# Optimization experiments

Hardware: AMD Instinct MI355X
Metric: run time of the kernel (lower is better)

## Reference

```python
import jax, jax.numpy as jnp
import numpy as np

B, N, E, Dh, L = 64, 128, 1024, 300, 2  # batch, num_utter, emb_dim, hidden_dim, gnn_layers


def gru_cell(x, h, wih, whh, bih, bhh):
    # torch.nn.GRUCell math; gate order r, z, n
    gi = x @ wih.T + bih
    gh = h @ whh.T + bhh
    ir, iz, inn = jnp.split(gi, 3, axis=-1)
    hr, hz, hn = jnp.split(gh, 3, axis=-1)
    r = jax.nn.sigmoid(ir + hr)
    z = jax.nn.sigmoid(iz + hz)
    n = jnp.tanh(inn + r * hn)
    return (1.0 - z) * n + z * h


def dag_layer(Hl, mask, wg, bg, cwih, cwhh, cbih, cbhh, pwih, pwhh, pbih, pbhh):
    # Hl: (B,N,Dh); mask: (B,N,N) strict-causal DAG adjacency (float 0/1)
    wq, wk = wg[:Dh], wg[Dh:]  # GatLinear: Linear(2*Dh, 1) split over [Q; K]
    x0 = Hl[:, 0]
    z0 = jnp.zeros_like(x0)
    C0 = gru_cell(x0, z0, cwih, cwhh, cbih, cbhh)  # grus_c(H0, hx=None)
    P0 = gru_cell(z0, x0, pwih, pwhh, pbih, pbhh)  # grus_p(M=0, H0)
    buf0 = jnp.zeros_like(Hl).at[:, 0].set(C0 + P0)

    xs = (jnp.swapaxes(Hl[:, 1:], 0, 1),      # (N-1,B,Dh)
          jnp.swapaxes(mask[:, 1:], 0, 1),    # (N-1,B,N)
          jnp.arange(1, Hl.shape[1]))

    def step(buf, inp):
        x, m, i = inp  # x:(B,Dh), m:(B,N) allows only positions j<i with adj==1
        alpha = (x @ wq)[:, None] + buf @ wk + bg        # (B,N) additive score
        alpha = alpha - (1.0 - m) * 1e30                 # mask_logic
        w = jax.nn.softmax(alpha, axis=-1)
        M = jnp.einsum('bn,bnd->bd', w, buf)             # attn_sum over history H1
        C = gru_cell(x, M, cwih, cwhh, cbih, cbhh)       # grus_c(H_i, M)
        P = gru_cell(M, x, pwih, pwhh, pbih, pbhh)       # grus_p(M, H_i)
        return buf.at[:, i].set(C + P), None

    buf, _ = jax.lax.scan(step, buf0, xs)
    return buf


def setup_inputs():
    key = jax.random.key(0)
    ks = jax.random.split(key, 16)
    features = jax.random.normal(ks[0], (B, N, E), jnp.float32)
    adj = jax.random.randint(ks[1], (B, N, N), 0, 2, dtype=jnp.int32)
    idx = jnp.arange(1, N)
    adj = adj.at[:, idx, idx - 1].set(1)  # every utterance links to its predecessor (valid DAG)
    s_mask = jax.random.randint(ks[2], (B, N, N), 0, 2, dtype=jnp.int32)
    s_mask_onehot = jax.nn.one_hot(s_mask, 2, dtype=jnp.int32)
    lengths = jnp.full((B,), N, dtype=jnp.int32)
    s = 0.05
    return {
        'features': features,
        'fc1_w': jax.random.normal(ks[3], (E, Dh), jnp.float32) * s,
        'fc1_b': jnp.zeros((Dh,), jnp.float32),
        'gat_w': jax.random.normal(ks[4], (L, 2 * Dh), jnp.float32) * s,
        'gat_b': jnp.zeros((L,), jnp.float32),
        'gc_wih': jax.random.normal(ks[5], (L, 3 * Dh, Dh), jnp.float32) * s,
        'gc_whh': jax.random.normal(ks[6], (L, 3 * Dh, Dh), jnp.float32) * s,
        'gc_bih': jnp.zeros((L, 3 * Dh), jnp.float32),
        'gc_bhh': jnp.zeros((L, 3 * Dh), jnp.float32),
        'gp_wih': jax.random.normal(ks[7], (L, 3 * Dh, Dh), jnp.float32) * s,
        'gp_whh': jax.random.normal(ks[8], (L, 3 * Dh, Dh), jnp.float32) * s,
        'gp_bih': jnp.zeros((L, 3 * Dh), jnp.float32),
        'gp_bhh': jnp.zeros((L, 3 * Dh), jnp.float32),
        'adj': adj,
        's_mask': s_mask,
        's_mask_onehot': s_mask_onehot,
        'lengths': lengths,
    }


def reference(features, fc1_w, fc1_b, gat_w, gat_b, gc_wih, gc_whh, gc_bih, gc_bhh,
              gp_wih, gp_whh, gp_bih, gp_bhh, adj, s_mask, s_mask_onehot, lengths):
    H0 = jax.nn.relu(features @ fc1_w + fc1_b)                 # (B,N,Dh)
    causal = jnp.tril(jnp.ones((N, N), features.dtype), k=-1)  # strictly past (j<i)
    mask = adj.astype(features.dtype) * causal                 # adj[:, i, :i]
    Hs = [H0]
    Hl = H0
    for l in range(L):
        Hl = dag_layer(Hl, mask, gat_w[l], gat_b[l],
                       gc_wih[l], gc_whh[l], gc_bih[l], gc_bhh[l],
                       gp_wih[l], gp_whh[l], gp_bih[l], gp_bhh[l])
        Hs.append(Hl)
    Hs.append(features)
    # nodal_att_type=None -> attentive_node_features is identity; module returns H
    return jnp.concatenate(Hs, axis=2)  # (B,N,Dh*(L+1)+E)
```

## Files before the change

kernel.cpp:

```cpp
#include <hip/hip_runtime.h>
#include <hip/hip_fp16.h>

#define B_   64
#define NB   128
#define E_   1024
#define DH   300
#define G3   900
#define G6   1800
#define OUTD 1924
#define SLICES 4
#define PK_STRIDE 1800
#define MROW 160
#define BROWS 1856

typedef _Float16 h2raw __attribute__((ext_vector_type(2)));

__device__ __forceinline__ float dot2f(unsigned int m2, unsigned int w, float acc) {
    h2raw a, b;
    __builtin_memcpy(&a, &m2, 4);
    __builtin_memcpy(&b, &w, 4);
    return __builtin_amdgcn_fdot2(a, b, acc, false);
}

__device__ __forceinline__ unsigned int packh2(float x, float y) {
    __half2 h;
    h.x = __float2half_rn(x);
    h.y = __float2half_rn(y);
    unsigned int u;
    __builtin_memcpy(&u, &h, 4);
    return u;
}

__device__ __forceinline__ float sigmoidf_(float x) { return 1.f / (1.f + __expf(-x)); }
__device__ __forceinline__ float tanh_fast(float x) { return 1.f - 2.f / (__expf(2.f * x) + 1.f); }

__global__ __launch_bounds__(256)
void copy_feat(const float* __restrict__ f, float* __restrict__ out) {
    const long id = (long)blockIdx.x * 256 + threadIdx.x;
    const long r = id >> 8;
    const int  c = (int)(id & 255);
    const float4 v = ((const float4*)(f + r * E_))[c];
    ((float4*)(out + r * OUTD + 3 * DH))[c] = v;
}

__global__ __launch_bounds__(256)
void pack2(const float* __restrict__ gc_whh, const float* __restrict__ gp_wih,
           unsigned int* __restrict__ dst) {
    const int id = blockIdx.x * 256 + threadIdx.x;
    if (id >= 2 * 150 * PK_STRIDE) return;
    const int l   = id / (150 * PK_STRIDE);
    const int rem = id % (150 * PK_STRIDE);
    const int kp  = rem / PK_STRIDE;
    const int R   = rem % PK_STRIDE;
    const int mat = R / G3;
    const int o   = R % G3;
    const float* W = (mat ? gp_wih : gc_whh) + (long)l * G3 * DH;
    const float2 v = *(const float2*)(W + (long)o * DH + 2 * kp);
    dst[id] = packh2(v.x, v.y);
}

__global__ __launch_bounds__(256)
void pack_af(const float* __restrict__ src, unsigned int* __restrict__ dst) {
    const long id = (long)blockIdx.x * 256 + threadIdx.x;
    const long r = id >> 9;
    const int kp = (int)(id & 511);
    const float2 v = *(const float2*)(src + r * E_ + 2 * kp);
    dst[id] = packh2(v.x, v.y);
}

__global__ __launch_bounds__(256)
void pack_bf(const float* __restrict__ W, unsigned int* __restrict__ dst) {
    const int id = blockIdx.x * 256 + threadIdx.x;
    const int n = id >> 9;
    const int kp = id & 511;
    unsigned int u = 0u;
    if (n < DH) u = packh2(W[(2 * kp) * DH + n], W[(2 * kp + 1) * DH + n]);
    dst[id] = u;
}

__global__ __launch_bounds__(256)
void pack_bw2(const float* __restrict__ Wc, const float* __restrict__ Wp,
              unsigned int* __restrict__ dst) {
    const int id = blockIdx.x * 256 + threadIdx.x;
    if (id >= 2 * BROWS * 160) return;
    const int l   = id / (BROWS * 160);
    const int rem = id % (BROWS * 160);
    const int n   = rem / 160;
    const int kp  = rem % 160;
    unsigned int u = 0u;
    if (n < G6 && kp < 150) {
        const float* W = (n < G3 ? Wc : Wp) + (long)l * G3 * DH;
        const int o = (n < G3) ? n : n - G3;
        const float2 v = *(const float2*)(W + (long)o * DH + 2 * kp);
        u = packh2(v.x, v.y);
    }
    dst[id] = u;
}

template<int RELU, int PACKOUT>
__global__ __launch_bounds__(256)
void gemm_h16(const unsigned int* __restrict__ APK, int ldap,
              const unsigned int* __restrict__ BPK, int ldbp,
              const float* __restrict__ bias1, const float* __restrict__ bias2, int bsplit,
              float* __restrict__ C, int ldc,
              unsigned int* __restrict__ CPK, int ldcp,
              int N, int KP)
{
    __shared__ __align__(16) unsigned int As[16][132];
    __shared__ __align__(16) unsigned int Bs[16][68];
    const int tid = threadIdx.x;
    const int m0 = blockIdx.y * 128;
    const int n0 = blockIdx.x * 64;
    const int tx = tid & 15, ty = tid >> 4;
    const int am = tid >> 1, ak8 = (tid & 1) * 8;
    const int bn = tid >> 2, bk4 = (tid & 3) * 4;

    float acc[8][4] = {{0.f}};
    const unsigned int* ap = APK + (long)(m0 + am) * ldap + ak8;
    const unsigned int* bp = BPK + (long)(n0 + bn) * ldbp + bk4;

    for (int kp0 = 0; kp0 < KP; kp0 += 16) {
        const uint4 a0 = *(const uint4*)(ap + kp0);
        const uint4 a1 = *(const uint4*)(ap + kp0 + 4);
        const uint4 bq = *(const uint4*)(bp + kp0);
        As[ak8 + 0][am] = a0.x; As[ak8 + 1][am] = a0.y;
        As[ak8 + 2][am] = a0.z; As[ak8 + 3][am] = a0.w;
        As[ak8 + 4][am] = a1.x; As[ak8 + 5][am] = a1.y;
        As[ak8 + 6][am] = a1.z; As[ak8 + 7][am] = a1.w;
        Bs[bk4 + 0][bn] = bq.x; Bs[bk4 + 1][bn] = bq.y;
        Bs[bk4 + 2][bn] = bq.z; Bs[bk4 + 3][bn] = bq.w;
        __syncthreads();
        #pragma unroll
        for (int kp = 0; kp < 16; ++kp) {
            const uint4 aA = *(const uint4*)&As[kp][ty * 8];
            const uint4 aB = *(const uint4*)&As[kp][ty * 8 + 4];
            const uint4 bb = *(const uint4*)&Bs[kp][tx * 4];
            const unsigned int av[8] = {aA.x, aA.y, aA.z, aA.w, aB.x, aB.y, aB.z, aB.w};
            const unsigned int bv[4] = {bb.x, bb.y, bb.z, bb.w};
            #pragma unroll
            for (int ii = 0; ii < 8; ++ii)
                #pragma unroll
                for (int jj = 0; jj < 4; ++jj)
                    acc[ii][jj] = dot2f(av[ii], bv[jj], acc[ii][jj]);
        }
        __syncthreads();
    }

    const int gn0 = n0 + tx * 4;
    #pragma unroll
    for (int ii = 0; ii < 8; ++ii) {
        const int gm = m0 + ty * 8 + ii;
        float* cp = C + (long)gm * ldc + gn0;
        if (gn0 + 3 < N) {
            const float* bb4 = (gn0 < bsplit) ? bias1 + gn0 : bias2 + (gn0 - bsplit);
            const float4 bb = *(const float4*)bb4;
            float4 o;
            o.x = acc[ii][0] + bb.x; o.y = acc[ii][1] + bb.y;
            o.z = acc[ii][2] + bb.z; o.w = acc[ii][3] + bb.w;
            if (RELU) { o.x = fmaxf(o.x, 0.f); o.y = fmaxf(o.y, 0.f); o.z = fmaxf(o.z, 0.f); o.w = fmaxf(o.w, 0.f); }
            *(float4*)cp = o;
            if (PACKOUT) {
                unsigned int* pk = CPK + (long)gm * ldcp + (gn0 >> 1);
                pk[0] = packh2(o.x, o.y);
                pk[1] = packh2(o.z, o.w);
            }
        } else if (gn0 < N) {
            for (int jj = 0; jj < 4; ++jj) {
                const int gn = gn0 + jj;
                if (gn < N) {
                    float v = acc[ii][jj] + ((gn < bsplit) ? bias1[gn] : bias2[gn - bsplit]);
                    if (RELU) v = fmaxf(v, 0.f);
                    cp[jj] = v;
                }
            }
        }
    }
}

__global__ __launch_bounds__(512, 2)
void scan14(float* __restrict__ out,
            const float* __restrict__ GG,
            const unsigned int* __restrict__ PK2L,
            const float* __restrict__ cbhh,
            const float* __restrict__ pbih,
            const int* __restrict__ adj,
            const float* __restrict__ wk,
            unsigned long long* __restrict__ TBL,
            unsigned int* __restrict__ APKN,
            int l)
{
    extern __shared__ unsigned int histp[];
    __shared__ float wsm2[NB];
    __shared__ float betas[NB];
    __shared__ float Mlds[DH];
    __shared__ __align__(16) unsigned int M2[152];
    __shared__ float gmv[456];
    __shared__ float mx2s, S_pres;

    const int tid = threadIdx.x;
    const int lane = tid & 63;
    const int wid = tid >> 6;
    const int b = blockIdx.x & 63;
    const int k = blockIdx.x >> 6;
    const int swk = (k == 3) ? 72 : 76;

    float* outb = out + (long)b * NB * OUTD;
    const float* xcol = outb + l * DH;
    float* ycol = outb + (l + 1) * DH;
    const float* ggb = GG + (long)b * NB * G6;
    const int* adjb = adj + b * NB * NB;
    unsigned long long* mb = TBL + (long)b * NB * MROW;
    unsigned int* mb32 = (unsigned int*)mb;

    if (tid < 152) M2[tid] = 0u;

    const int D = 76 * k + ((tid < swk) ? tid : 0);
    const float cb0 = cbhh[D], cb1 = cbhh[DH + D], cb2 = cbhh[2 * DH + D];
    const float pb0 = pbih[D], pb1 = pbih[DH + D], pb2 = pbih[2 * DH + D];
    const float wkD = wk[D];

    const int ROWS = 6 * swk;
    int R;
    {
        const int t = (tid < ROWS) ? tid : 0;
        const int d = t % swk;
        const int r = t / swk;
        R = (r / 3) * G3 + (r % 3) * DH + 76 * k + d;
    }
    unsigned int w[152];
    #pragma unroll
    for (int j = 0; j < 150; ++j) w[j] = PK2L[j * PK_STRIDE + R];
    w[150] = 0u; w[151] = 0u;

    __syncthreads();

    const bool isv = (tid >= 256) && (tid < 406);
    const int vt = tid - 256;

    for (int i = 0; i < NB; ++i) {
        float gi0 = 0, gi1 = 0, gi2 = 0, gp0 = 0, gp1 = 0, gp2 = 0, xi = 0;
        if (tid < swk) {
            const float* gic = ggb + (long)i * G6;
            gi0 = gic[D]; gi1 = gic[DH + D]; gi2 = gic[2 * DH + D];
            gp0 = gic[G3 + D]; gp1 = gic[G3 + DH + D]; gp2 = gic[G3 + 2 * DH + D];
            xi = xcol[(long)i * OUTD + D];
        }
        int a0p = 0, a1p = 0;
        if (wid == 2 && i + 1 < NB) {
            a0p = adjb[(i + 1) * NB + lane];
            a1p = adjb[(i + 1) * NB + 64 + lane];
        }

        if (i > 0) {
            float V0 = 0.f, V1 = 0.f;
            if (wid == 0) {
                const unsigned long long* trow = mb + (long)(i - 1) * MROW;
                const unsigned int tag = (unsigned int)i;
                const bool act = (lane < 8);
                unsigned long long tv = 0;
                while (true) {
                    if (act && (unsigned int)tv != tag)
                        tv = __hip_atomic_load(&trow[152 + lane],
                                               __ATOMIC_RELAXED, __HIP_MEMORY_SCOPE_AGENT);
                    if (__all(!act || (unsigned int)tv == tag)) break;
                }
                unsigned long long d0 = 0, d1 = 0;
                if (lane < 38) {
                    d0 = __hip_atomic_load(&trow[2 * lane],
                                           __ATOMIC_RELAXED, __HIP_MEMORY_SCOPE_AGENT);
                    d1 = __hip_atomic_load(&trow[2 * lane + 1],
                                           __ATOMIC_RELAXED, __HIP_MEMORY_SCOPE_AGENT);
                }
                float bp = 0.f;
                if (act) {
                    const unsigned int hb = (unsigned int)(tv >> 32);
                    __builtin_memcpy(&bp, &hb, 4);
                }
                bp += __shfl_xor(bp, 1);
                bp += __shfl_xor(bp, 2);
                bp += __shfl_xor(bp, 4);
                if (lane == 0) betas[i - 1] = __shfl(bp, 0);

                if (lane < 38) {
                    uint4 q;
                    q.x = (unsigned int)d0; q.y = (unsigned int)(d0 >> 32);
                    q.z = (unsigned int)d1; q.w = (unsigned int)(d1 >> 32);
                    *(uint4*)&histp[(i - 1) * 152 + 4 * lane] = q;
                }
            } else if (isv) {
                #pragma unroll 4
                for (int j = 0; j + 1 < i; ++j) {
                    const float wj = wsm2[j];
                    const unsigned int u = histp[j * 152 + vt];
                    __half2 h; __builtin_memcpy(&h, &u, 4);
                    V0 = fmaf(wj, __half2float(h.x), V0);
                    V1 = fmaf(wj, __half2float(h.y), V1);
                }
            }
            __syncthreads();

            if (isv) {
                const float beta_new = betas[i - 1];
                const float mxl = mx2s;
                float S = S_pres, e;
                if (beta_new > mxl) {
                    const float sc = __expf(mxl - beta_new);
                    V0 *= sc; V1 *= sc; S *= sc; e = 1.f;
                } else {
                    e = __expf(beta_new - mxl);
                }
                const unsigned int u = histp[(i - 1) * 152 + vt];
                __half2 h; __builtin_memcpy(&h, &u, 4);
                S += e;
                V0 = fmaf(e, __half2float(h.x), V0);
                V1 = fmaf(e, __half2float(h.y), V1);
                const float inv = 1.f / S;
                const float m0 = V0 * inv, m1 = V1 * inv;
                Mlds[2 * vt] = m0;
                Mlds[2 * vt + 1] = m1;
                M2[vt] = packh2(m0, m1);
            }
        } else {
            if (tid < DH) Mlds[tid] = 0.f;
        }
        __syncthreads();

        if (tid < ROWS) {
            float a0 = 0.f, a1 = 0.f;
            #pragma unroll
            for (int j4 = 0; j4 < 152; j4 += 4) {
                const uint4 m4 = *(const uint4*)&M2[j4];
                a0 = dot2f(m4.x, w[j4 + 0], a0);
                a1 = dot2f(m4.y, w[j4 + 1], a1);
                a0 = dot2f(m4.z, w[j4 + 2], a0);
                a1 = dot2f(m4.w, w[j4 + 3], a1);
            }
            gmv[tid] = a0 + a1;
        }
        __syncthreads();

        if (wid < 2) {
            float rowv = 0.f;
            if (tid < swk) {
                const float Mi = Mlds[D];
                const float hc0 = gmv[0 * swk + tid] + cb0;
                const float hc1 = gmv[1 * swk + tid] + cb1;
                const float hc2 = gmv[2 * swk + tid] + cb2;
                const float rc = sigmoidf_(gi0 + hc0);
                const float zc = sigmoidf_(gi1 + hc1);
                const float nc = tanh_fast(gi2 + rc * hc2);
                const float Cc = (1.f - zc) * nc + zc * Mi;
                const float ip0 = gmv[3 * swk + tid] + pb0;
                const float ip1 = gmv[4 * swk + tid] + pb1;
                const float ip2 = gmv[5 * swk + tid] + pb2;
                const float rp = sigmoidf_(ip0 + gp0);
                const float zp = sigmoidf_(ip1 + gp1);
                const float np = tanh_fast(ip2 + rp * gp2);
                const float Pp = (1.f - zp) * np + zp * xi;
                rowv = Cc + Pp;
            }
            const float pr = __shfl_xor(rowv, 1);
            const unsigned int pairu32 = packh2(rowv, pr);
            if (tid < swk && !(tid & 1)) {
                __hip_atomic_store(&mb32[(long)i * (MROW * 2) + 38 * k + (tid >> 1)], pairu32,
                                   __ATOMIC_RELAXED, __HIP_MEMORY_SCOPE_AGENT);
                if (l == 0)
                    APKN[((long)b * NB + i) * 160 + 38 * k + (tid >> 1)] = pairu32;
            }
            float bv = (tid < swk) ? rowv * wkD : 0.f;
            #pragma unroll
            for (int off = 32; off; off >>= 1) bv += __shfl_xor(bv, off);
            asm volatile("s_waitcnt vmcnt(0)" ::: "memory");
            if (lane == 0) {
                unsigned int bbits;
                __builtin_memcpy(&bbits, &bv, 4);
                const unsigned long long pkt =
                    ((unsigned long long)bbits << 32) | (unsigned int)(i + 1);
                __hip_atomic_store(&mb[(long)i * MROW + 152 + 2 * k + wid], pkt,
                                   __ATOMIC_RELAXED, __HIP_MEMORY_SCOPE_AGENT);
            }
            if (tid < swk) ycol[(long)i * OUTD + D] = rowv;
        } else if (wid == 2 && i + 1 < NB) {
            const int j1 = lane + 64;
            const bool v0 = (lane < i) && (a0p != 0);
            const bool v1 = (j1 < i) && (a1p != 0);
            const float aa0 = v0 ? betas[lane] : -3.0e38f;
            const float aa1 = v1 ? betas[j1]   : -3.0e38f;
            float mx = fmaxf(aa0, aa1);
            #pragma unroll
            for (int off = 32; off; off >>= 1) mx = fmaxf(mx, __shfl_xor(mx, off));
            const float e0 = v0 ? __expf(aa0 - mx) : 0.f;
            const float e1 = v1 ? __expf(aa1 - mx) : 0.f;
            float s = e0 + e1;
            #pragma unroll
            for (int off = 32; off; off >>= 1) s += __shfl_xor(s, off);
            wsm2[lane] = e0;
            wsm2[j1]   = e1;
            if (lane == 0) { mx2s = mx; S_pres = s; }
        }
        __syncthreads();
    }
}

extern "C" void kernel_launch(void* const* d_in, const int* in_sizes, int n_in,
                              void* d_out, int out_size, void* d_ws, size_t ws_size,
                              hipStream_t stream) {
    (void)in_sizes; (void)n_in; (void)out_size; (void)ws_size;
    const float* features = (const float*)d_in[0];
    const float* fc1_w    = (const float*)d_in[1];
    const float* fc1_b    = (const float*)d_in[2];
    const float* gat_w    = (const float*)d_in[3];
    const float* gc_wih   = (const float*)d_in[5];
    const float* gc_whh   = (const float*)d_in[6];
    const float* gc_bih   = (const float*)d_in[7];
    const float* gc_bhh   = (const float*)d_in[8];
    const float* gp_wih   = (const float*)d_in[9];
    const float* gp_whh   = (const float*)d_in[10];
    const float* gp_bih   = (const float*)d_in[11];
    const float* gp_bhh   = (const float*)d_in[12];
    const int*   adj      = (const int*)d_in[13];
    float* out = (float*)d_out;

    unsigned long long* TB = (unsigned long long*)d_ws;
    float* GG = (float*)(TB + 2L * B_ * NB * MROW);
    unsigned int* PK2  = (unsigned int*)(GG + 8192L * G6);
    unsigned int* APK2 = PK2 + 2 * 150 * PK_STRIDE;
    unsigned int* BPKF = APK2 + 8192L * 160;
    unsigned int* BPKL = BPKF + 320L * 512;
    unsigned int* APK1 = (unsigned int*)GG;

    hipFuncSetAttribute(reinterpret_cast<const void*>(scan14),
                        hipFuncAttributeMaxDynamicSharedMemorySize, 80000);
    hipMemsetAsync(TB, 0, 2L * B_ * NB * MROW * sizeof(unsigned long long), stream);
    hipMemsetAsync(APK2, 0, 8192L * 160 * sizeof(unsigned int), stream);

    copy_feat<<<dim3((B_ * NB * E_) / 1024), 256, 0, stream>>>(features, out);
    pack2<<<dim3((2 * 150 * PK_STRIDE + 255) / 256), 256, 0, stream>>>(gc_whh, gp_wih, PK2);

    pack_af<<<dim3(8192 * 512 / 256), 256, 0, stream>>>(features, APK1);
    pack_bf<<<dim3(320 * 512 / 256), 256, 0, stream>>>(fc1_w, BPKF);
    pack_bw2<<<dim3((2 * BROWS * 160 + 255) / 256), 256, 0, stream>>>(gc_wih, gp_whh, BPKL);

    gemm_h16<1, 1><<<dim3(5, 64), 256, 0, stream>>>(
        APK1, 512, BPKF, 512, fc1_b, fc1_b, DH, out, OUTD, APK2, 160, DH, 512);

    for (int l = 0; l < 2; ++l) {
        gemm_h16<0, 0><<<dim3(29, 64), 256, 0, stream>>>(
            APK2, 160, BPKL + (long)l * BROWS * 160, 160,
            gc_bih + l * G3, gp_bhh + l * G3, G3,
            GG, G6, (unsigned int*)nullptr, 0, G6, 160);
        scan14<<<dim3(SLICES * B_), 512, 77824, stream>>>(
            out, GG, PK2 + (long)l * 150 * PK_STRIDE,
            gc_bhh + l * G3, gp_bih + l * G3, adj,
            gat_w + l * 2 * DH + DH,
            TB + (long)l * B_ * NB * MROW,
            APK2, l);
    }
}
```

Baseline: 1.174 ms.

## Replace dot2 FMA GEMM with MFMA 16x16x32 f16 matrix-core GEMM

Rewrites the packed-half GEMM used for the input projection and the per-layer GRU input gates. It drops the shared-memory-tiled fdot2 kernel and uses MFMA f16 intrinsics, with each wave computing a 32x64 tile and loading fragments straight from global memory. The goal is to move GEMM throughput onto the matrix cores. The cost is no LDS staging, so global loads are more redundant, and the epilogue now does scalar stores with a shuffle to pack the half output.

```diff
diff --git a/kernel.cpp b/kernel.cpp
--- a/kernel.cpp
+++ b/kernel.cpp
@@ -14,6 +14,8 @@
 #define BROWS 1856
 
 typedef _Float16 h2raw __attribute__((ext_vector_type(2)));
+typedef _Float16 f16x8 __attribute__((ext_vector_type(8)));
+typedef float f32x4 __attribute__((ext_vector_type(4)));
 
 __device__ __forceinline__ float dot2f(unsigned int m2, unsigned int w, float acc) {
     h2raw a, b;
@@ -97,80 +99,74 @@
     dst[id] = u;
 }
 
+__device__ __forceinline__ f16x8 ldfrag(const unsigned int* p) {
+    const uint4 u = *(const uint4*)p;
+    f16x8 r;
+    __builtin_memcpy(&r, &u, 16);
+    return r;
+}
+
 template<int RELU, int PACKOUT>
 __global__ __launch_bounds__(256)
-void gemm_h16(const unsigned int* __restrict__ APK, int ldap,
-              const unsigned int* __restrict__ BPK, int ldbp,
-              const float* __restrict__ bias1, const float* __restrict__ bias2, int bsplit,
-              float* __restrict__ C, int ldc,
-              unsigned int* __restrict__ CPK, int ldcp,
-              int N, int KP)
+void gemm_mf(const unsigned int* __restrict__ APK, int ldap,
+             const unsigned int* __restrict__ BPK, int ldbp,
+             const float* __restrict__ bias1, const float* __restrict__ bias2, int bsplit,
+             float* __restrict__ C, int ldc,
+             unsigned int* __restrict__ CPK, int ldcp,
+             int N, int KSTEPS)
 {
-    __shared__ __align__(16) unsigned int As[16][132];
-    __shared__ __align__(16) unsigned int Bs[16][68];
-    const int tid = threadIdx.x;
-    const int m0 = blockIdx.y * 128;
+    const int lane = threadIdx.x & 63;
+    const int wv = threadIdx.x >> 6;
+    const int m0 = blockIdx.y * 128 + wv * 32;
     const int n0 = blockIdx.x * 64;
-    const int tx = tid & 15, ty = tid >> 4;
-    const int am = tid >> 1, ak8 = (tid & 1) * 8;
-    const int bn = tid >> 2, bk4 = (tid & 3) * 4;
-
-    float acc[8][4] = {{0.f}};
-    const unsigned int* ap = APK + (long)(m0 + am) * ldap + ak8;
-    const unsigned int* bp = BPK + (long)(n0 + bn) * ldbp + bk4;
-
-    for (int kp0 = 0; kp0 < KP; kp0 += 16) {
-        const uint4 a0 = *(const uint4*)(ap + kp0);
-        const uint4 a1 = *(const uint4*)(ap + kp0 + 4);
-        const uint4 bq = *(const uint4*)(bp + kp0);
-        As[ak8 + 0][am] = a0.x; As[ak8 + 1][am] = a0.y;
-        As[ak8 + 2][am] = a0.z; As[ak8 + 3][am] = a0.w;
-        As[ak8 + 4][am] = a1.x; As[ak8 + 5][am] = a1.y;
-        As[ak8 + 6][am] = a1.z; As[ak8 + 7][am] = a1.w;
-        Bs[bk4 + 0][bn] = bq.x; Bs[bk4 + 1][bn] = bq.y;
-        Bs[bk4 + 2][bn] = bq.z; Bs[bk4 + 3][bn] = bq.w;
-        __syncthreads();
+    const int ln = lane & 15;
+    const int lh = lane >> 4;
+
+    const unsigned int* a0p = APK + (long)(m0 + ln) * ldap + lh * 4;
+    const unsigned int* a1p = a0p + 16L * ldap;
+    const unsigned int* b0p = BPK + (long)(n0 + ln) * ldbp + lh * 4;
+
+    f32x4 acc[2][4];
+    #pragma unroll
+    for (int mi = 0; mi < 2; ++mi)
         #pragma unroll
-        for (int kp = 0; kp < 16; ++kp) {
-            const uint4 aA = *(const uint4*)&As[kp][ty * 8];
-            const uint4 aB = *(const uint4*)&As[kp][ty * 8 + 4];
-            const uint4 bb = *(const uint4*)&Bs[kp][tx * 4];
-            const unsigned int av[8] = {aA.x, aA.y, aA.z, aA.w, aB.x, aB.y, aB.z, aB.w};
-            const unsigned int bv[4] = {bb.x, bb.y, bb.z, bb.w};
+        for (int bj = 0; bj < 4; ++bj)
+            acc[mi][bj] = (f32x4){0.f, 0.f, 0.f, 0.f};
+
+    for (int ks = 0; ks < KSTEPS; ++ks) {
+        const int off = ks * 16;
+        const f16x8 a0 = ldfrag(a0p + off);
+        const f16x8 a1 = ldfrag(a1p + off);
+        const f16x8 b0 = ldfrag(b0p + off);
+        const f16x8 b1 = ldfrag(b0p + 16L * ldbp + off);
+        const f16x8 b2 = ldfrag(b0p + 32L * ldbp + off);
+        const f16x8 b3 = ldfrag(b0p + 48L * ldbp + off);
+        acc[0][0] = __builtin_amdgcn_mfma_f32_16x16x32_f16(a0, b0, acc[0][0], 0, 0, 0);
+        acc[0][1] = __builtin_amdgcn_mfma_f32_16x16x32_f16(a0, b1, acc[0][1], 0, 0, 0);
+        acc[0][2] = __builtin_amdgcn_mfma_f32_16x16x32_f16(a0, b2, acc[0][2], 0, 0, 0);
+        acc[0][3] = __builtin_amdgcn_mfma_f32_16x16x32_f16(a0, b3, acc[0][3], 0, 0, 0);
+        acc[1][0] = __builtin_amdgcn_mfma_f32_16x16x32_f16(a1, b0, acc[1][0], 0, 0, 0);
+        acc[1][1] = __builtin_amdgcn_mfma_f32_16x16x32_f16(a1, b1, acc[1][1], 0, 0, 0);
+        acc[1][2] = __builtin_amdgcn_mfma_f32_16x16x32_f16(a1, b2, acc[1][2], 0, 0, 0);
+        acc[1][3] = __builtin_amdgcn_mfma_f32_16x16x32_f16(a1, b3, acc[1][3], 0, 0, 0);
+    }
+
+    #pragma unroll
+    for (int mi = 0; mi < 2; ++mi) {
+        #pragma unroll
+        for (int bj = 0; bj < 4; ++bj) {
+            const int gcol = n0 + bj * 16 + ln;
             #pragma unroll
-            for (int ii = 0; ii < 8; ++ii)
-                #pragma unroll
-                for (int jj = 0; jj < 4; ++jj)
-                    acc[ii][jj] = dot2f(av[ii], bv[jj], acc[ii][jj]);
-        }
-        __syncthreads();
-    }
-
-    const int gn0 = n0 + tx * 4;
-    #pragma unroll
-    for (int ii = 0; ii < 8; ++ii) {
-        const int gm = m0 + ty * 8 + ii;
-        float* cp = C + (long)gm * ldc + gn0;
-        if (gn0 + 3 < N) {
-            const float* bb4 = (gn0 < bsplit) ? bias1 + gn0 : bias2 + (gn0 - bsplit);
-            const float4 bb = *(const float4*)bb4;
-            float4 o;
-            o.x = acc[ii][0] + bb.x; o.y = acc[ii][1] + bb.y;
-            o.z = acc[ii][2] + bb.z; o.w = acc[ii][3] + bb.w;
-            if (RELU) { o.x = fmaxf(o.x, 0.f); o.y = fmaxf(o.y, 0.f); o.z = fmaxf(o.z, 0.f); o.w = fmaxf(o.w, 0.f); }
-            *(float4*)cp = o;
-            if (PACKOUT) {
-                unsigned int* pk = CPK + (long)gm * ldcp + (gn0 >> 1);
-                pk[0] = packh2(o.x, o.y);
-                pk[1] = packh2(o.z, o.w);
-            }
-        } else if (gn0 < N) {
-            for (int jj = 0; jj < 4; ++jj) {
-                const int gn = gn0 + jj;
-                if (gn < N) {
-                    float v = acc[ii][jj] + ((gn < bsplit) ? bias1[gn] : bias2[gn - bsplit]);
-                    if (RELU) v = fmaxf(v, 0.f);
-                    cp[jj] = v;
+            for (int r = 0; r < 4; ++r) {
+                const int gm = m0 + mi * 16 + lh * 4 + r;
+                float v = acc[mi][bj][r];
+                if (gcol < N) v += (gcol < bsplit) ? bias1[gcol] : bias2[gcol - bsplit];
+                if (RELU) v = fmaxf(v, 0.f);
+                const float pr = PACKOUT ? __shfl_xor(v, 1) : 0.f;
+                if (gcol < N) {
+                    C[(long)gm * ldc + gcol] = v;
+                    if (PACKOUT && !(ln & 1))
+                        CPK[(long)gm * ldcp + (gcol >> 1)] = packh2(v, pr);
                 }
             }
         }
@@ -441,14 +437,14 @@
     pack_bf<<<dim3(320 * 512 / 256), 256, 0, stream>>>(fc1_w, BPKF);
     pack_bw2<<<dim3((2 * BROWS * 160 + 255) / 256), 256, 0, stream>>>(gc_wih, gp_whh, BPKL);
 
-    gemm_h16<1, 1><<<dim3(5, 64), 256, 0, stream>>>(
-        APK1, 512, BPKF, 512, fc1_b, fc1_b, DH, out, OUTD, APK2, 160, DH, 512);
+    gemm_mf<1, 1><<<dim3(5, 64), 256, 0, stream>>>(
+        APK1, 512, BPKF, 512, fc1_b, fc1_b, DH, out, OUTD, APK2, 160, DH, 32);
 
     for (int l = 0; l < 2; ++l) {
-        gemm_h16<0, 0><<<dim3(29, 64), 256, 0, stream>>>(
+        gemm_mf<0, 0><<<dim3(29, 64), 256, 0, stream>>>(
             APK2, 160, BPKL + (long)l * BROWS * 160, 160,
             gc_bih + l * G3, gp_bhh + l * G3, G3,
-            GG, G6, (unsigned int*)nullptr, 0, G6, 160);
+            GG, G6, (unsigned int*)nullptr, 0, G6, 10);
         scan14<<<dim3(SLICES * B_), 512, 77824, stream>>>(
             out, GG, PK2 + (long)l * 150 * PK_STRIDE,
             gc_bhh + l * G3, gp_bih + l * G3, adj,
```

Result: faster. 1.099 ms (-6.4%).
